# Kernel optimization log

Hardware: AMD Instinct MI355X
Metric: run time of the kernel (lower is better)

Reference implementation:

```python
import jax, jax.numpy as jnp
import numpy as np

# Fano plane lines (1-indexed as in the torch module), converted to 0-indexed
# gather indices into the 7 imaginary channels.
FANO_LINES = [(1, 2, 3), (1, 4, 5), (1, 6, 7), (2, 4, 6), (2, 5, 7), (3, 4, 7), (3, 5, 6)]
LINE_IDX = np.array([[i - 1 for i in line] for line in FANO_LINES])  # [7, 3]


def setup_inputs() -> dict:
    key = jax.random.key(0)
    k1, k2 = jax.random.split(key)
    B, N = 8, 2048
    o = jax.random.normal(k1, (B, N, 8), dtype=jnp.float32)
    # nn.Parameter(torch.ones(7) / 7); perturb slightly so softmax is non-trivial
    line_weights = jnp.ones((7,), dtype=jnp.float32) / 7.0 \
        + 0.01 * jax.random.normal(k2, (7,), dtype=jnp.float32)
    return {"o": o, "line_weights": line_weights}


def reference(o, line_weights):
    # o: [B, N, 8] = real (ch 0) + 7 imaginary channels
    real = o[:, :, 0:1]            # [B, N, 1]
    imag = o[:, :, 1:]             # [B, N, 7]; q = k = v = imag

    # torch.einsum('bni,bmj->bnm', q_line, k_line) sums i and j independently:
    # line score = (sum_i q_line[b,n,i]) * (sum_j k_line[b,m,j]).
    line_sums = imag[:, :, LINE_IDX].sum(axis=-1)       # [B, N, 7] per-line channel sums

    w = jax.nn.softmax(line_weights)                    # [7]
    # weighted stack then mean over 7 lines, fused as one contraction
    scores = jnp.einsum('bnl,bml->bnm', line_sums * w, line_sums) / 7.0  # [B, N, N]

    attn = jax.nn.softmax(scores, axis=-1)              # [B, N, N]
    # dropout is identity at inference
    out_imag = jnp.einsum('bnm,bmd->bnd', attn, imag)   # [B, N, 7]

    out = jnp.concatenate([real, out_imag], axis=-1)    # [B, N, 8]
    norm = jnp.linalg.norm(out, axis=-1, keepdims=True)
    return out / (norm + 1e-15)
```

## Files before the change

### kernel.cpp

```cpp
#include <hip/hip_runtime.h>
#include <math.h>

#define NB 8
#define NN 2048
#define NTHREADS 512
#define SPLIT 32
#define RPT 4
#define ROWS_PER_BLOCK 64
#define LOG2E 1.44269504088896340736f

#if defined(__has_builtin)
#  if __has_builtin(__builtin_amdgcn_exp2f)
#    define EXP2F(x) __builtin_amdgcn_exp2f(x)
#  else
#    define EXP2F(x) exp2f(x)
#  endif
#else
#  define EXP2F(x) exp2f(x)
#endif

__global__ __launch_bounds__(NTHREADS, 2)
void fano_attn_kernel(const float* __restrict__ o,
                      const float* __restrict__ lw,
                      float* __restrict__ out) {
    __shared__ float sV[3][NN][2];
    __shared__ float sV3[NN];

    const int tid = threadIdx.x;
    const int t   = tid & (SPLIT - 1);
    const int g   = tid >> 5;
    const int b   = blockIdx.x >> 5;
    const int rowbase = (blockIdx.x & 31) * ROWS_PER_BLOCK;
    const float* obatch = o + (size_t)b * (NN * 8);

    float w[7];
    {
        float e[7]; float se = 0.f;
#pragma unroll
        for (int l = 0; l < 7; ++l) { e[l] = __expf(lw[l]); se += e[l]; }
        const float inv = LOG2E / (7.0f * se);
#pragma unroll
        for (int l = 0; l < 7; ++l) w[l] = e[l] * inv;
    }

    float4 qr0[RPT], qr1[RPT];
#pragma unroll
    for (int k = 0; k < RPT; ++k) {
        const float* row = obatch + (size_t)(rowbase + g * RPT + k) * 8;
        qr0[k] = *(const float4*)row;
        qr1[k] = *(const float4*)(row + 4);
    }

#pragma unroll
    for (int j = 0; j < NN / NTHREADS; ++j) {
        const int m = tid + j * NTHREADS;
        const float* row = obatch + (size_t)m * 8;
        const float4 a0 = *(const float4*)row;
        const float4 a1 = *(const float4*)(row + 4);
        *(float2*)&sV[0][m][0] = make_float2(a0.y, a0.z);
        *(float2*)&sV[1][m][0] = make_float2(a0.w, a1.x);
        *(float2*)&sV[2][m][0] = make_float2(a1.y, a1.z);
        sV3[m] = a1.w;
    }

    float qa[RPT][7], realp[RPT];
#pragma unroll
    for (int k = 0; k < RPT; ++k) {
        realp[k] = qr0[k].x;
        const float i0 = qr0[k].y, i1 = qr0[k].z, i2 = qr0[k].w;
        const float i3 = qr1[k].x, i4 = qr1[k].y, i5 = qr1[k].z, i6 = qr1[k].w;
        const float q0 = (i0 + i1 + i2) * w[0];
        const float q1 = (i0 + i3 + i4) * w[1];
        const float q2 = (i0 + i5 + i6) * w[2];
        const float q3 = (i1 + i3 + i5) * w[3];
        const float q4 = (i1 + i4 + i6) * w[4];
        const float q5 = (i2 + i3 + i6) * w[5];
        const float q6 = (i2 + i4 + i5) * w[6];
        qa[k][0] = q0 + q1 + q2;
        qa[k][1] = q0 + q3 + q4;
        qa[k][2] = q0 + q5 + q6;
        qa[k][3] = q1 + q3 + q5;
        qa[k][4] = q1 + q4 + q6;
        qa[k][5] = q2 + q3 + q6;
        qa[k][6] = q2 + q4 + q5;
    }

    float acc[RPT][7];
    float psum[RPT];
#pragma unroll
    for (int k = 0; k < RPT; ++k) {
        psum[k] = 0.f;
#pragma unroll
        for (int d = 0; d < 7; ++d) acc[k][d] = 0.f;
    }

    __syncthreads();

#pragma unroll 4
    for (int i = 0; i < NN / SPLIT; ++i) {
        const int m = i * SPLIT + t;
        const float2 va = *(const float2*)&sV[0][m][0];
        const float2 vb = *(const float2*)&sV[1][m][0];
        const float2 vc = *(const float2*)&sV[2][m][0];
        const float  vd = sV3[m];
#pragma unroll
        for (int k = 0; k < RPT; ++k) {
            float s = qa[k][0] * va.x;
            s = fmaf(qa[k][1], va.y, s);
            s = fmaf(qa[k][2], vb.x, s);
            s = fmaf(qa[k][3], vb.y, s);
            s = fmaf(qa[k][4], vc.x, s);
            s = fmaf(qa[k][5], vc.y, s);
            s = fmaf(qa[k][6], vd,   s);
            const float p = EXP2F(s);
            psum[k] += p;
            acc[k][0] = fmaf(p, va.x, acc[k][0]);
            acc[k][1] = fmaf(p, va.y, acc[k][1]);
            acc[k][2] = fmaf(p, vb.x, acc[k][2]);
            acc[k][3] = fmaf(p, vb.y, acc[k][3]);
            acc[k][4] = fmaf(p, vc.x, acc[k][4]);
            acc[k][5] = fmaf(p, vc.y, acc[k][5]);
            acc[k][6] = fmaf(p, vd,   acc[k][6]);
        }
    }

#pragma unroll
    for (int ofs = 1; ofs < SPLIT; ofs <<= 1) {
#pragma unroll
        for (int k = 0; k < RPT; ++k) {
            psum[k] += __shfl_xor(psum[k], ofs);
#pragma unroll
            for (int d = 0; d < 7; ++d)
                acc[k][d] += __shfl_xor(acc[k][d], ofs);
        }
    }

    if (t == 0) {
#pragma unroll
        for (int k = 0; k < RPT; ++k) {
            const float invs = 1.0f / psum[k];
            float oi[7];
            float n2 = realp[k] * realp[k];
#pragma unroll
            for (int d = 0; d < 7; ++d) {
                oi[d] = acc[k][d] * invs;
                n2 += oi[d] * oi[d];
            }
            const float scale = 1.0f / (sqrtf(n2) + 1e-15f);
            float4 r0, r1;
            r0.x = realp[k] * scale; r0.y = oi[0] * scale;
            r0.z = oi[1] * scale;    r0.w = oi[2] * scale;
            r1.x = oi[3] * scale;    r1.y = oi[4] * scale;
            r1.z = oi[5] * scale;    r1.w = oi[6] * scale;
            float* orow = out + ((size_t)(b * NN + rowbase + g * RPT + k)) * 8;
            *(float4*)orow       = r0;
            *(float4*)(orow + 4) = r1;
        }
    }
}

extern "C" void kernel_launch(void* const* d_in, const int* in_sizes, int n_in,
                              void* d_out, int out_size, void* d_ws, size_t ws_size,
                              hipStream_t stream) {
    const float* o  = (const float*)d_in[0];
    const float* lw = (const float*)d_in[1];
    float* out      = (float*)d_out;
    const int grid = NB * (NN / ROWS_PER_BLOCK);
    fano_attn_kernel<<<dim3(grid), dim3(NTHREADS), 0, stream>>>(o, lw, out);
}
```

Measured before the change: 76.51 us.

## Vectorize score/accumulate with packed float2 math and widen key split to 64

Rewrites the inner score and accumulation FMAs as two-wide vector operations so the compiler can emit packed FP32 instructions (v_pk_fma_f32) on CDNA. SPLIT goes from 32 to 64, so each wavefront covers one row group across the keys, rows per block drop to 32 and the grid doubles. The occupancy hint is raised to 4 blocks per CU. The trade-off is a longer shuffle reduction and twice as many blocks each restaging the full V into LDS.

```diff
diff --git a/kernel.cpp b/kernel.cpp
--- a/kernel.cpp
+++ b/kernel.cpp
@@ -4,10 +4,13 @@
 #define NB 8
 #define NN 2048
 #define NTHREADS 512
-#define SPLIT 32
+#define SPLIT 64
 #define RPT 4
-#define ROWS_PER_BLOCK 64
+#define ROWS_PER_BLOCK ((NTHREADS / SPLIT) * RPT)
+#define BLOCKS_PER_BATCH (NN / ROWS_PER_BLOCK)
 #define LOG2E 1.44269504088896340736f
+
+typedef float v2f __attribute__((ext_vector_type(2)));
 
 #if defined(__has_builtin)
 #  if __has_builtin(__builtin_amdgcn_exp2f)
@@ -19,7 +22,7 @@
 #  define EXP2F(x) exp2f(x)
 #endif
 
-__global__ __launch_bounds__(NTHREADS, 2)
+__global__ __launch_bounds__(NTHREADS, 4)
 void fano_attn_kernel(const float* __restrict__ o,
                       const float* __restrict__ lw,
                       float* __restrict__ out) {
@@ -27,10 +30,10 @@
     __shared__ float sV3[NN];
 
     const int tid = threadIdx.x;
-    const int t   = tid & (SPLIT - 1);
-    const int g   = tid >> 5;
-    const int b   = blockIdx.x >> 5;
-    const int rowbase = (blockIdx.x & 31) * ROWS_PER_BLOCK;
+    const int t   = tid % SPLIT;
+    const int g   = tid / SPLIT;
+    const int b   = blockIdx.x / BLOCKS_PER_BATCH;
+    const int rowbase = (blockIdx.x % BLOCKS_PER_BATCH) * ROWS_PER_BLOCK;
     const float* obatch = o + (size_t)b * (NN * 8);
 
     float w[7];
@@ -63,7 +66,8 @@
         sV3[m] = a1.w;
     }
 
-    float qa[RPT][7], realp[RPT];
+    v2f qa01[RPT], qa23[RPT], qa45[RPT];
+    float qa6[RPT], realp[RPT];
 #pragma unroll
     for (int k = 0; k < RPT; ++k) {
         realp[k] = qr0[k].x;
@@ -76,22 +80,19 @@
         const float q4 = (i1 + i4 + i6) * w[4];
         const float q5 = (i2 + i3 + i6) * w[5];
         const float q6 = (i2 + i4 + i5) * w[6];
-        qa[k][0] = q0 + q1 + q2;
-        qa[k][1] = q0 + q3 + q4;
-        qa[k][2] = q0 + q5 + q6;
-        qa[k][3] = q1 + q3 + q5;
-        qa[k][4] = q1 + q4 + q6;
-        qa[k][5] = q2 + q3 + q6;
-        qa[k][6] = q2 + q4 + q5;
+        qa01[k] = (v2f){q0 + q1 + q2, q0 + q3 + q4};
+        qa23[k] = (v2f){q0 + q5 + q6, q1 + q3 + q5};
+        qa45[k] = (v2f){q1 + q4 + q6, q2 + q3 + q6};
+        qa6[k]  = q2 + q4 + q5;
     }
 
-    float acc[RPT][7];
-    float psum[RPT];
+    v2f accv[RPT][3];
+    float acc6[RPT], psum[RPT];
 #pragma unroll
     for (int k = 0; k < RPT; ++k) {
-        psum[k] = 0.f;
+        psum[k] = 0.f; acc6[k] = 0.f;
 #pragma unroll
-        for (int d = 0; d < 7; ++d) acc[k][d] = 0.f;
+        for (int j = 0; j < 3; ++j) accv[k][j] = (v2f){0.f, 0.f};
     }
 
     __syncthreads();
@@ -99,28 +100,21 @@
 #pragma unroll 4
     for (int i = 0; i < NN / SPLIT; ++i) {
         const int m = i * SPLIT + t;
-        const float2 va = *(const float2*)&sV[0][m][0];
-        const float2 vb = *(const float2*)&sV[1][m][0];
-        const float2 vc = *(const float2*)&sV[2][m][0];
-        const float  vd = sV3[m];
+        const v2f  va = *(const v2f*)&sV[0][m][0];
+        const v2f  vb = *(const v2f*)&sV[1][m][0];
+        const v2f  vc = *(const v2f*)&sV[2][m][0];
+        const float vd = sV3[m];
 #pragma unroll
         for (int k = 0; k < RPT; ++k) {
-            float s = qa[k][0] * va.x;
-            s = fmaf(qa[k][1], va.y, s);
-            s = fmaf(qa[k][2], vb.x, s);
-            s = fmaf(qa[k][3], vb.y, s);
-            s = fmaf(qa[k][4], vc.x, s);
-            s = fmaf(qa[k][5], vc.y, s);
-            s = fmaf(qa[k][6], vd,   s);
+            const v2f d = qa01[k] * va + qa23[k] * vb + qa45[k] * vc;
+            const float s = fmaf(qa6[k], vd, d.x + d.y);
             const float p = EXP2F(s);
             psum[k] += p;
-            acc[k][0] = fmaf(p, va.x, acc[k][0]);
-            acc[k][1] = fmaf(p, va.y, acc[k][1]);
-            acc[k][2] = fmaf(p, vb.x, acc[k][2]);
-            acc[k][3] = fmaf(p, vb.y, acc[k][3]);
-            acc[k][4] = fmaf(p, vc.x, acc[k][4]);
-            acc[k][5] = fmaf(p, vc.y, acc[k][5]);
-            acc[k][6] = fmaf(p, vd,   acc[k][6]);
+            const v2f p2 = (v2f){p, p};
+            accv[k][0] = p2 * va + accv[k][0];
+            accv[k][1] = p2 * vb + accv[k][1];
+            accv[k][2] = p2 * vc + accv[k][2];
+            acc6[k] = fmaf(p, vd, acc6[k]);
         }
     }
 
@@ -130,8 +124,11 @@
         for (int k = 0; k < RPT; ++k) {
             psum[k] += __shfl_xor(psum[k], ofs);
 #pragma unroll
-            for (int d = 0; d < 7; ++d)
-                acc[k][d] += __shfl_xor(acc[k][d], ofs);
+            for (int j = 0; j < 3; ++j) {
+                accv[k][j].x += __shfl_xor(accv[k][j].x, ofs);
+                accv[k][j].y += __shfl_xor(accv[k][j].y, ofs);
+            }
+            acc6[k] += __shfl_xor(acc6[k], ofs);
         }
     }
 
@@ -139,12 +136,13 @@
 #pragma unroll
         for (int k = 0; k < RPT; ++k) {
             const float invs = 1.0f / psum[k];
-            float oi[7];
+            float oi[7] = { accv[k][0].x, accv[k][0].y, accv[k][1].x,
+                            accv[k][1].y, accv[k][2].x, accv[k][2].y, acc6[k] };
             float n2 = realp[k] * realp[k];
 #pragma unroll
             for (int d = 0; d < 7; ++d) {
-                oi[d] = acc[k][d] * invs;
-                n2 += oi[d] * oi[d];
+                oi[d] *= invs;
+                n2 = fmaf(oi[d], oi[d], n2);
             }
             const float scale = 1.0f / (sqrtf(n2) + 1e-15f);
             float4 r0, r1;
@@ -165,6 +163,6 @@
     const float* o  = (const float*)d_in[0];
     const float* lw = (const float*)d_in[1];
     float* out      = (float*)d_out;
-    const int grid = NB * (NN / ROWS_PER_BLOCK);
+    const int grid = NB * BLOCKS_PER_BATCH;
     fano_attn_kernel<<<dim3(grid), dim3(NTHREADS), 0, stream>>>(o, lw, out);
 }
```

Measured after the change: 75.66 us. Within noise of the previous version (-1.1%).
